# Kernel tuning notes

Hardware: AMD Instinct MI355X
Metric: run time of the kernel (lower is better)

Reference implementation:

```python
import jax, jax.numpy as jnp
import numpy as np

IN_CH = 256
OUT_CH = 256
RED = 4
QK = OUT_CH // RED  # 64


def setup_inputs() -> dict:
    key = jax.random.key(0)
    ks = jax.random.split(key, 7)
    s = 1.0 / np.sqrt(IN_CH)
    return {
        "x": jax.random.normal(ks[0], (8, IN_CH, 64, 64), dtype=jnp.float32),
        "w_q": jax.random.uniform(ks[1], (QK, IN_CH), jnp.float32, -s, s),
        "b_q": jax.random.uniform(ks[2], (QK,), jnp.float32, -s, s),
        "w_k": jax.random.uniform(ks[3], (QK, IN_CH), jnp.float32, -s, s),
        "b_k": jax.random.uniform(ks[4], (QK,), jnp.float32, -s, s),
        "w_v": jax.random.uniform(ks[5], (OUT_CH, IN_CH), jnp.float32, -s, s),
        "b_v": jax.random.uniform(ks[6], (OUT_CH,), jnp.float32, -s, s),
    }


def reference(x, w_q, b_q, w_k, b_k, w_v, b_v):
    B, C, H, W = x.shape
    xt = x.reshape(B, C, H * W)  # [B, C, N]
    # 1x1 convs == channel matmuls
    q = jnp.einsum('dc,bcn->bnd', w_q, xt) + b_q  # [B, N, QK]
    k = jnp.einsum('dc,bcn->bdn', w_k, xt) + b_k[:, None]  # [B, QK, N]
    v = jnp.einsum('dc,bcn->bnd', w_v, xt) + b_v  # [B, N, OUT]
    scores = jnp.einsum('bnd,bdm->bnm', q, k)  # [B, N, N], no scaling (as in source)
    attn = jax.nn.softmax(scores, axis=-1)
    out = jnp.einsum('bnm,bmd->bdn', attn, v)  # [B, OUT, N]
    return out.reshape(B, -1, H, W)
```

## Files before the change

### kernel.cpp

```cpp
#include <hip/hip_runtime.h>

typedef __bf16 bf16x8 __attribute__((ext_vector_type(8)));
typedef __bf16 bf16x2 __attribute__((ext_vector_type(2)));
typedef float f32x4 __attribute__((ext_vector_type(4)));
typedef unsigned int u32;
typedef u32 u32x4v __attribute__((ext_vector_type(4)));
typedef unsigned short u16;

#define LOG2E 1.44269504088896f

__device__ __forceinline__ u32 pk2(float a, float b){
  bf16x2 v; v[0] = (__bf16)a; v[1] = (__bf16)b;
  return __builtin_bit_cast(u32, v);
}

__global__ void prep_w(const float* __restrict__ wq, const float* __restrict__ wk,
                       const float* __restrict__ wv, u16* __restrict__ wfrag){
  int idx  = blockIdx.x * 256 + threadIdx.x;
  int e    = idx & 7;
  int lane = (idx >> 3) & 63;
  int f    = idx >> 9;
  int cc = f / 24, dt = f % 24;
  int d = dt * 16 + (lane & 15);
  int c = cc * 32 + (lane >> 4) * 8 + e;
  float v;
  if (d < 64)       v = wq[d * 256 + c];
  else if (d < 128) v = wk[(d - 64) * 256 + c];
  else              v = wv[(d - 128) * 256 + c];
  __bf16 h = (__bf16)v;
  wfrag[idx] = __builtin_bit_cast(u16, h);
}

__launch_bounds__(512, 4)
__global__ void proj_kernel(const float* __restrict__ x,
                            const float* __restrict__ bq, const float* __restrict__ bk,
                            const float* __restrict__ bv,
                            const u16* __restrict__ wfrag,
                            u16* __restrict__ qb, u16* __restrict__ kb, u16* __restrict__ vt)
{
  __shared__ u16 xlds[64 * 256];
  const int b    = blockIdx.x & 7;
  const int n0   = (blockIdx.x >> 3) * 64;
  const int t    = threadIdx.x;
  const int lane = t & 63;
  const int w    = t >> 6;
  const int g    = lane >> 4, j = lane & 15;

  {
    const int n  = t & 63;
    const int ch = t >> 6;
    const float* xp = x + ((size_t)b * 256) * 4096 + n0 + n;
    char* lbase = reinterpret_cast<char*>(xlds);
    #pragma unroll
    for (int pass = 0; pass < 4; ++pass){
      int c = pass * 64 + ch * 8;
      float f0 = xp[(size_t)(c+0)*4096], f1 = xp[(size_t)(c+1)*4096];
      float f2 = xp[(size_t)(c+2)*4096], f3 = xp[(size_t)(c+3)*4096];
      float f4 = xp[(size_t)(c+4)*4096], f5 = xp[(size_t)(c+5)*4096];
      float f6 = xp[(size_t)(c+6)*4096], f7 = xp[(size_t)(c+7)*4096];
      uint4 q;
      q.x = pk2(f0, f1); q.y = pk2(f2, f3); q.z = pk2(f4, f5); q.w = pk2(f6, f7);
      u32 off = (u32)n * 512 + (((u32)c * 2) ^ (((u32)n & 31) << 4));
      *reinterpret_cast<uint4*>(lbase + off) = q;
    }
  }
  __syncthreads();

  f32x4 acc[3][4];
  #pragma unroll
  for (int i = 0; i < 3; ++i)
    #pragma unroll
    for (int nt = 0; nt < 4; ++nt) acc[i][nt] = f32x4{0.f,0.f,0.f,0.f};

  const char* lbase = reinterpret_cast<const char*>(xlds);
  for (int cc = 0; cc < 8; ++cc){
    bf16x8 a[3];
    #pragma unroll
    for (int i = 0; i < 3; ++i)
      a[i] = *reinterpret_cast<const bf16x8*>(wfrag + ((size_t)(cc*24 + w*3 + i) * 64 + lane) * 8);
    bf16x8 bb[4];
    #pragma unroll
    for (int nt = 0; nt < 4; ++nt){
      const u32 row = nt * 16 + j;
      const u32 off = row * 512 + (((u32)(cc * 64 + g * 16)) ^ ((row & 31) << 4));
      bb[nt] = *reinterpret_cast<const bf16x8*>(lbase + off);
    }
    #pragma unroll
    for (int i = 0; i < 3; ++i)
      #pragma unroll
      for (int nt = 0; nt < 4; ++nt)
        acc[i][nt] = __builtin_amdgcn_mfma_f32_16x16x32_bf16(a[i], bb[nt], acc[i][nt], 0, 0, 0);
  }

  #pragma unroll
  for (int i = 0; i < 3; ++i){
    const int dt = w * 3 + i;
    const int d0 = dt * 16;
    const int dd = d0 + 4 * g;
    if (d0 < 64){
      float b0 = bq[dd], b1 = bq[dd+1], b2 = bq[dd+2], b3 = bq[dd+3];
      #pragma unroll
      for (int nt = 0; nt < 4; ++nt){
        const int n = n0 + nt * 16 + j;
        uint2 u;
        u.x = pk2((acc[i][nt][0] + b0) * LOG2E, (acc[i][nt][1] + b1) * LOG2E);
        u.y = pk2((acc[i][nt][2] + b2) * LOG2E, (acc[i][nt][3] + b3) * LOG2E);
        *reinterpret_cast<uint2*>(qb + ((size_t)b * 4096 + n) * 64 + dd) = u;
      }
    } else if (d0 < 128){
      const int dk = dd - 64;
      float b0 = bk[dk], b1 = bk[dk+1], b2 = bk[dk+2], b3 = bk[dk+3];
      #pragma unroll
      for (int nt = 0; nt < 4; ++nt){
        const int n = n0 + nt * 16 + j;
        uint2 u;
        u.x = pk2(acc[i][nt][0] + b0, acc[i][nt][1] + b1);
        u.y = pk2(acc[i][nt][2] + b2, acc[i][nt][3] + b3);
        *reinterpret_cast<uint2*>(kb + ((size_t)b * 4096 + n) * 64 + dk) = u;
      }
    } else {
      const int dv = dd - 128;
      float b0 = bv[dv], b1 = bv[dv+1], b2 = bv[dv+2], b3 = bv[dv+3];
      #pragma unroll
      for (int nt = 0; nt < 4; ++nt){
        const int scol = ((nt & 2) << 4) | ((j & 12) << 1) | ((nt & 1) << 2) | (j & 3);
        const int n = n0 + scol;
        u16* vp = vt + (size_t)b * 256 * 4096 + n;
        __bf16 h0 = (__bf16)(acc[i][nt][0] + b0);
        __bf16 h1 = (__bf16)(acc[i][nt][1] + b1);
        __bf16 h2 = (__bf16)(acc[i][nt][2] + b2);
        __bf16 h3 = (__bf16)(acc[i][nt][3] + b3);
        vp[(size_t)(dv+0) * 4096] = __builtin_bit_cast(u16, h0);
        vp[(size_t)(dv+1) * 4096] = __builtin_bit_cast(u16, h1);
        vp[(size_t)(dv+2) * 4096] = __builtin_bit_cast(u16, h2);
        vp[(size_t)(dv+3) * 4096] = __builtin_bit_cast(u16, h3);
      }
    }
  }
}

__launch_bounds__(512, 4)
__global__ void attn_kernel(const u16* __restrict__ qb, const u16* __restrict__ kb,
                            const u16* __restrict__ vt, float* __restrict__ out)
{
  __shared__ u16 kl[2][64 * 64];
  __shared__ u16 vl[2][256 * 64];

  const int b    = blockIdx.x & 7;
  const int qc   = blockIdx.x >> 3;
  const int t    = threadIdx.x, lane = t & 63, w = t >> 6;
  const int g    = lane >> 4, j = lane & 15;
  const int colq = w & 3;
  const int dvh  = (w >> 2) * 128;

  const u16* Kg = kb + (size_t)b * 4096 * 64;
  const u16* Vg = vt + (size_t)b * 256 * 4096;

  const u16* Qrow = qb + ((size_t)b * 4096 + qc * 64 + colq * 16 + j) * 64;
  const bf16x8 qf0 = *reinterpret_cast<const bf16x8*>(Qrow + 8 * g);
  const bf16x8 qf1 = *reinterpret_cast<const bf16x8*>(Qrow + 32 + 8 * g);

  f32x4 o[8];
  #pragma unroll
  for (int i = 0; i < 8; ++i) o[i] = f32x4{0.f,0.f,0.f,0.f};
  float mrun = -1.0e30f, lrun = 0.f;

  auto stage = [&](int tile, int buf){
    const int m0 = tile * 64;
    {
      const int r = w * 8 + (lane >> 3);
      const char* src = reinterpret_cast<const char*>(Kg + (size_t)(m0 + r) * 64)
                        + ((((u32)lane & 7) * 16) ^ ((((u32)r) & 7) << 4));
      char* dst = reinterpret_cast<char*>(&kl[buf][0]) + w * 1024;
      __builtin_amdgcn_global_load_lds((const __attribute__((address_space(1))) void*)src,
                                       (__attribute__((address_space(3))) void*)dst, 16, 0, 0);
    }
    #pragma unroll
    for (int i = 0; i < 4; ++i){
      const int dv = i * 64 + w * 8 + (lane >> 3);
      const char* src = reinterpret_cast<const char*>(Vg + (size_t)dv * 4096 + m0)
                        + ((((u32)lane & 7) * 16) ^ (((u32)dv & 7) << 4));
      char* dst = reinterpret_cast<char*>(&vl[buf][0]) + i * 8192 + w * 1024;
      __builtin_amdgcn_global_load_lds((const __attribute__((address_space(1))) void*)src,
                                       (__attribute__((address_space(3))) void*)dst, 16, 0, 0);
    }
  };

  stage(0, 0);
  __syncthreads();

  const u32 vsw = ((u32)j & 7) << 4;

  for (int tile = 0; tile < 64; ++tile){
    const int cur = tile & 1;
    if (tile + 1 < 64) stage(tile + 1, cur ^ 1);

    const char* kbase = reinterpret_cast<const char*>(&kl[cur][0]);
    const char* vbase = reinterpret_cast<const char*>(&vl[cur][0]);

    f32x4 s[4];
    __builtin_amdgcn_s_setprio(1);
    #pragma unroll
    for (int mt = 0; mt < 4; ++mt){
      const u32 row = mt * 16 + j;
      const u32 sw  = (row & 7) << 4;
      bf16x8 ka0 = *reinterpret_cast<const bf16x8*>(kbase + row * 128 + (((u32)(g * 16)) ^ sw));
      bf16x8 ka1 = *reinterpret_cast<const bf16x8*>(kbase + row * 128 + (((u32)(64 + g * 16)) ^ sw));
      f32x4 z = f32x4{0.f,0.f,0.f,0.f};
      z = __builtin_amdgcn_mfma_f32_16x16x32_bf16(ka0, qf0, z, 0, 0, 0);
      z = __builtin_amdgcn_mfma_f32_16x16x32_bf16(ka1, qf1, z, 0, 0, 0);
      s[mt] = z;
    }
    __builtin_amdgcn_s_setprio(0);

    float pmax = s[0][0];
    #pragma unroll
    for (int mt = 0; mt < 4; ++mt)
      #pragma unroll
      for (int r = 0; r < 4; ++r) pmax = fmaxf(pmax, s[mt][r]);
    pmax = fmaxf(pmax, __shfl_xor(pmax, 16));
    pmax = fmaxf(pmax, __shfl_xor(pmax, 32));

    if (__any(pmax > mrun + 8.0f)){
      const float mnew  = fmaxf(mrun, pmax);
      const float alpha = __builtin_amdgcn_exp2f(mrun - mnew);
      mrun = mnew;
      lrun *= alpha;
      #pragma unroll
      for (int i = 0; i < 8; ++i){
        o[i][0] *= alpha; o[i][1] *= alpha; o[i][2] *= alpha; o[i][3] *= alpha;
      }
    }

    float psum = 0.f;
    u32 pw[8];
    #pragma unroll
    for (int mt = 0; mt < 4; ++mt){
      float p0 = __builtin_amdgcn_exp2f(s[mt][0] - mrun);
      float p1 = __builtin_amdgcn_exp2f(s[mt][1] - mrun);
      float p2 = __builtin_amdgcn_exp2f(s[mt][2] - mrun);
      float p3 = __builtin_amdgcn_exp2f(s[mt][3] - mrun);
      psum += (p0 + p1) + (p2 + p3);
      pw[2*mt]   = pk2(p0, p1);
      pw[2*mt+1] = pk2(p2, p3);
    }
    psum += __shfl_xor(psum, 16);
    psum += __shfl_xor(psum, 32);
    lrun += psum;

    __builtin_amdgcn_s_setprio(1);
    #pragma unroll
    for (int mc = 0; mc < 2; ++mc){
      u32x4v pv = { pw[4*mc+0], pw[4*mc+1], pw[4*mc+2], pw[4*mc+3] };
      bf16x8 pf = __builtin_bit_cast(bf16x8, pv);
      #pragma unroll
      for (int dt = 0; dt < 8; ++dt){
        const u32 dv = dvh + dt * 16 + j;
        bf16x8 vf = *reinterpret_cast<const bf16x8*>(vbase + dv * 128 + (((u32)(mc * 64 + 16 * g)) ^ vsw));
        o[dt] = __builtin_amdgcn_mfma_f32_16x16x32_bf16(vf, pf, o[dt], 0, 0, 0);
      }
    }
    __builtin_amdgcn_s_setprio(0);

    __syncthreads();
  }

  const float rinv = 1.0f / lrun;
  const int n = qc * 64 + colq * 16 + j;
  float* ob = out + (size_t)b * 256 * 4096 + n;
  #pragma unroll
  for (int dt = 0; dt < 8; ++dt){
    const int dv0 = dvh + dt * 16 + 4 * g;
    #pragma unroll
    for (int r = 0; r < 4; ++r)
      ob[(size_t)(dv0 + r) * 4096] = o[dt][r] * rinv;
  }
}

extern "C" void kernel_launch(void* const* d_in, const int* in_sizes, int n_in,
                              void* d_out, int out_size, void* d_ws, size_t ws_size,
                              hipStream_t stream)
{
  (void)in_sizes; (void)n_in; (void)out_size; (void)ws_size;
  const float* x  = (const float*)d_in[0];
  const float* wq = (const float*)d_in[1];
  const float* bq = (const float*)d_in[2];
  const float* wk = (const float*)d_in[3];
  const float* bk = (const float*)d_in[4];
  const float* wv = (const float*)d_in[5];
  const float* bv = (const float*)d_in[6];
  float* out = (float*)d_out;

  char* ws = (char*)d_ws;
  u16* qbuf  = (u16*)(ws + 0);
  u16* kbuf  = (u16*)(ws + 4194304);
  u16* vbuf  = (u16*)(ws + 8388608);
  u16* wfrag = (u16*)(ws + 25165824);

  prep_w<<<dim3(384), dim3(256), 0, stream>>>(wq, wk, wv, wfrag);
  proj_kernel<<<dim3(512), dim3(512), 0, stream>>>(x, bq, bk, bv, wfrag, qbuf, kbuf, vbuf);
  attn_kernel<<<dim3(512), dim3(512), 0, stream>>>(qbuf, kbuf, vbuf, out);
}
```

Measured before the change: 228.8 us.

## Switch attention kernel to 32x32x16 MFMA tiles with four waves per block

Rewrites the attention kernel to use 32x32x16 bf16 MFMAs instead of 16x16x32. Each of four waves now owns 32 query columns by 128 value channels, where before eight waves each owned 16 columns. The V column permutation written by the projection kernel is changed to match the new P fragment layout. The aim is higher MFMA throughput per instruction and fewer LDS fragment reads per FLOP, at the cost of more accumulator registers per thread and fewer waves per block.

```diff
diff --git a/kernel.cpp b/kernel.cpp
--- a/kernel.cpp
+++ b/kernel.cpp
@@ -3,6 +3,7 @@
 typedef __bf16 bf16x8 __attribute__((ext_vector_type(8)));
 typedef __bf16 bf16x2 __attribute__((ext_vector_type(2)));
 typedef float f32x4 __attribute__((ext_vector_type(4)));
+typedef float f32x16 __attribute__((ext_vector_type(16)));
 typedef unsigned int u32;
 typedef u32 u32x4v __attribute__((ext_vector_type(4)));
 typedef unsigned short u16;
@@ -123,7 +124,7 @@
       float b0 = bv[dv], b1 = bv[dv+1], b2 = bv[dv+2], b3 = bv[dv+3];
       #pragma unroll
       for (int nt = 0; nt < 4; ++nt){
-        const int scol = ((nt & 2) << 4) | ((j & 12) << 1) | ((nt & 1) << 2) | (j & 3);
+        const int scol = (nt << 4) | ((j & 8) >> 1) | ((j & 4) << 1) | (j & 3);
         const int n = n0 + scol;
         u16* vp = vt + (size_t)b * 256 * 4096 + n;
         __bf16 h0 = (__bf16)(acc[i][nt][0] + b0);
@@ -139,7 +140,7 @@
   }
 }
 
-__launch_bounds__(512, 4)
+__launch_bounds__(256, 2)
 __global__ void attn_kernel(const u16* __restrict__ qb, const u16* __restrict__ kb,
                             const u16* __restrict__ vt, float* __restrict__ out)
 {
@@ -149,38 +150,43 @@
   const int b    = blockIdx.x & 7;
   const int qc   = blockIdx.x >> 3;
   const int t    = threadIdx.x, lane = t & 63, w = t >> 6;
-  const int g    = lane >> 4, j = lane & 15;
-  const int colq = w & 3;
-  const int dvh  = (w >> 2) * 128;
+  const int i32l = lane & 31, hi = lane >> 5;
+  const int colg = w & 1;
+  const int dvh  = (w >> 1) * 128;
 
   const u16* Kg = kb + (size_t)b * 4096 * 64;
   const u16* Vg = vt + (size_t)b * 256 * 4096;
 
-  const u16* Qrow = qb + ((size_t)b * 4096 + qc * 64 + colq * 16 + j) * 64;
-  const bf16x8 qf0 = *reinterpret_cast<const bf16x8*>(Qrow + 8 * g);
-  const bf16x8 qf1 = *reinterpret_cast<const bf16x8*>(Qrow + 32 + 8 * g);
-
-  f32x4 o[8];
-  #pragma unroll
-  for (int i = 0; i < 8; ++i) o[i] = f32x4{0.f,0.f,0.f,0.f};
+  const u16* Qrow = qb + ((size_t)b * 4096 + qc * 64 + colg * 32 + i32l) * 64;
+  bf16x8 qf[4];
+  #pragma unroll
+  for (int kc = 0; kc < 4; ++kc)
+    qf[kc] = *reinterpret_cast<const bf16x8*>(Qrow + kc * 16 + hi * 8);
+
+  f32x16 o[4];
+  #pragma unroll
+  for (int ds = 0; ds < 4; ++ds)
+    #pragma unroll
+    for (int r = 0; r < 16; ++r) o[ds][r] = 0.f;
   float mrun = -1.0e30f, lrun = 0.f;
 
   auto stage = [&](int tile, int buf){
     const int m0 = tile * 64;
-    {
-      const int r = w * 8 + (lane >> 3);
+    #pragma unroll
+    for (int i = 0; i < 2; ++i){
+      const int r = i * 32 + w * 8 + (lane >> 3);
       const char* src = reinterpret_cast<const char*>(Kg + (size_t)(m0 + r) * 64)
                         + ((((u32)lane & 7) * 16) ^ ((((u32)r) & 7) << 4));
-      char* dst = reinterpret_cast<char*>(&kl[buf][0]) + w * 1024;
+      char* dst = reinterpret_cast<char*>(&kl[buf][0]) + i * 4096 + w * 1024;
       __builtin_amdgcn_global_load_lds((const __attribute__((address_space(1))) void*)src,
                                        (__attribute__((address_space(3))) void*)dst, 16, 0, 0);
     }
     #pragma unroll
-    for (int i = 0; i < 4; ++i){
-      const int dv = i * 64 + w * 8 + (lane >> 3);
+    for (int i = 0; i < 8; ++i){
+      const int dv = i * 32 + w * 8 + (lane >> 3);
       const char* src = reinterpret_cast<const char*>(Vg + (size_t)dv * 4096 + m0)
                         + ((((u32)lane & 7) * 16) ^ (((u32)dv & 7) << 4));
-      char* dst = reinterpret_cast<char*>(&vl[buf][0]) + i * 8192 + w * 1024;
+      char* dst = reinterpret_cast<char*>(&vl[buf][0]) + i * 4096 + w * 1024;
       __builtin_amdgcn_global_load_lds((const __attribute__((address_space(1))) void*)src,
                                        (__attribute__((address_space(3))) void*)dst, 16, 0, 0);
     }
@@ -189,7 +195,8 @@
   stage(0, 0);
   __syncthreads();
 
-  const u32 vsw = ((u32)j & 7) << 4;
+  const u32 swk   = ((u32)i32l & 7) << 4;
+  const u32 r0off = (u32)i32l * 128;
 
   for (int tile = 0; tile < 64; ++tile){
     const int cur = tile & 1;
@@ -198,27 +205,26 @@
     const char* kbase = reinterpret_cast<const char*>(&kl[cur][0]);
     const char* vbase = reinterpret_cast<const char*>(&vl[cur][0]);
 
-    f32x4 s[4];
+    f32x16 s0, s1;
+    #pragma unroll
+    for (int r = 0; r < 16; ++r){ s0[r] = 0.f; s1[r] = 0.f; }
     __builtin_amdgcn_s_setprio(1);
     #pragma unroll
-    for (int mt = 0; mt < 4; ++mt){
-      const u32 row = mt * 16 + j;
-      const u32 sw  = (row & 7) << 4;
-      bf16x8 ka0 = *reinterpret_cast<const bf16x8*>(kbase + row * 128 + (((u32)(g * 16)) ^ sw));
-      bf16x8 ka1 = *reinterpret_cast<const bf16x8*>(kbase + row * 128 + (((u32)(64 + g * 16)) ^ sw));
-      f32x4 z = f32x4{0.f,0.f,0.f,0.f};
-      z = __builtin_amdgcn_mfma_f32_16x16x32_bf16(ka0, qf0, z, 0, 0, 0);
-      z = __builtin_amdgcn_mfma_f32_16x16x32_bf16(ka1, qf1, z, 0, 0, 0);
-      s[mt] = z;
+    for (int kc = 0; kc < 4; ++kc){
+      const u32 cb = ((u32)(kc * 32 + hi * 16)) ^ swk;
+      bf16x8 ka0 = *reinterpret_cast<const bf16x8*>(kbase + r0off + cb);
+      bf16x8 ka1 = *reinterpret_cast<const bf16x8*>(kbase + 4096 + r0off + cb);
+      s0 = __builtin_amdgcn_mfma_f32_32x32x16_bf16(ka0, qf[kc], s0, 0, 0, 0);
+      s1 = __builtin_amdgcn_mfma_f32_32x32x16_bf16(ka1, qf[kc], s1, 0, 0, 0);
     }
     __builtin_amdgcn_s_setprio(0);
 
-    float pmax = s[0][0];
-    #pragma unroll
-    for (int mt = 0; mt < 4; ++mt)
-      #pragma unroll
-      for (int r = 0; r < 4; ++r) pmax = fmaxf(pmax, s[mt][r]);
-    pmax = fmaxf(pmax, __shfl_xor(pmax, 16));
+    float mx[8];
+    #pragma unroll
+    for (int r = 0; r < 8; ++r)
+      mx[r] = fmaxf(fmaxf(s0[r], s0[r+8]), fmaxf(s1[r], s1[r+8]));
+    float pmax = fmaxf(fmaxf(fmaxf(mx[0],mx[1]), fmaxf(mx[2],mx[3])),
+                       fmaxf(fmaxf(mx[4],mx[5]), fmaxf(mx[6],mx[7])));
     pmax = fmaxf(pmax, __shfl_xor(pmax, 32));
 
     if (__any(pmax > mrun + 8.0f)){
@@ -227,53 +233,57 @@
       mrun = mnew;
       lrun *= alpha;
       #pragma unroll
-      for (int i = 0; i < 8; ++i){
-        o[i][0] *= alpha; o[i][1] *= alpha; o[i][2] *= alpha; o[i][3] *= alpha;
+      for (int ds = 0; ds < 4; ++ds)
+        #pragma unroll
+        for (int r = 0; r < 16; ++r) o[ds][r] *= alpha;
+    }
+
+    float p0[16], p1[16];
+    #pragma unroll
+    for (int r = 0; r < 16; ++r){
+      p0[r] = __builtin_amdgcn_exp2f(s0[r] - mrun);
+      p1[r] = __builtin_amdgcn_exp2f(s1[r] - mrun);
+    }
+    float a8[8];
+    #pragma unroll
+    for (int r = 0; r < 8; ++r) a8[r] = (p0[r] + p0[r+8]) + (p1[r] + p1[r+8]);
+    float ps = ((a8[0]+a8[1]) + (a8[2]+a8[3])) + ((a8[4]+a8[5]) + (a8[6]+a8[7]));
+    ps += __shfl_xor(ps, 32);
+    lrun += ps;
+
+    u32x4v w0 = { pk2(p0[0],p0[1]),  pk2(p0[2],p0[3]),  pk2(p0[4],p0[5]),  pk2(p0[6],p0[7]) };
+    u32x4v w1 = { pk2(p0[8],p0[9]),  pk2(p0[10],p0[11]),pk2(p0[12],p0[13]),pk2(p0[14],p0[15]) };
+    u32x4v w2 = { pk2(p1[0],p1[1]),  pk2(p1[2],p1[3]),  pk2(p1[4],p1[5]),  pk2(p1[6],p1[7]) };
+    u32x4v w3 = { pk2(p1[8],p1[9]),  pk2(p1[10],p1[11]),pk2(p1[12],p1[13]),pk2(p1[14],p1[15]) };
+    bf16x8 pf[4] = { __builtin_bit_cast(bf16x8, w0), __builtin_bit_cast(bf16x8, w1),
+                     __builtin_bit_cast(bf16x8, w2), __builtin_bit_cast(bf16x8, w3) };
+
+    __builtin_amdgcn_s_setprio(1);
+    #pragma unroll
+    for (int c = 0; c < 4; ++c){
+      const u32 cb = ((u32)(c * 32 + hi * 16)) ^ swk;
+      #pragma unroll
+      for (int ds = 0; ds < 4; ++ds){
+        const u32 voff = (u32)(dvh + ds * 32) * 128 + r0off + cb;
+        bf16x8 vf = *reinterpret_cast<const bf16x8*>(vbase + voff);
+        o[ds] = __builtin_amdgcn_mfma_f32_32x32x16_bf16(vf, pf[c], o[ds], 0, 0, 0);
       }
     }
-
-    float psum = 0.f;
-    u32 pw[8];
-    #pragma unroll
-    for (int mt = 0; mt < 4; ++mt){
-      float p0 = __builtin_amdgcn_exp2f(s[mt][0] - mrun);
-      float p1 = __builtin_amdgcn_exp2f(s[mt][1] - mrun);
-      float p2 = __builtin_amdgcn_exp2f(s[mt][2] - mrun);
-      float p3 = __builtin_amdgcn_exp2f(s[mt][3] - mrun);
-      psum += (p0 + p1) + (p2 + p3);
-      pw[2*mt]   = pk2(p0, p1);
-      pw[2*mt+1] = pk2(p2, p3);
-    }
-    psum += __shfl_xor(psum, 16);
-    psum += __shfl_xor(psum, 32);
-    lrun += psum;
-
-    __builtin_amdgcn_s_setprio(1);
-    #pragma unroll
-    for (int mc = 0; mc < 2; ++mc){
-      u32x4v pv = { pw[4*mc+0], pw[4*mc+1], pw[4*mc+2], pw[4*mc+3] };
-      bf16x8 pf = __builtin_bit_cast(bf16x8, pv);
-      #pragma unroll
-      for (int dt = 0; dt < 8; ++dt){
-        const u32 dv = dvh + dt * 16 + j;
-        bf16x8 vf = *reinterpret_cast<const bf16x8*>(vbase + dv * 128 + (((u32)(mc * 64 + 16 * g)) ^ vsw));
-        o[dt] = __builtin_amdgcn_mfma_f32_16x16x32_bf16(vf, pf, o[dt], 0, 0, 0);
-      }
-    }
     __builtin_amdgcn_s_setprio(0);
 
     __syncthreads();
   }
 
   const float rinv = 1.0f / lrun;
-  const int n = qc * 64 + colq * 16 + j;
+  const int n = qc * 64 + colg * 32 + i32l;
   float* ob = out + (size_t)b * 256 * 4096 + n;
   #pragma unroll
-  for (int dt = 0; dt < 8; ++dt){
-    const int dv0 = dvh + dt * 16 + 4 * g;
-    #pragma unroll
-    for (int r = 0; r < 4; ++r)
-      ob[(size_t)(dv0 + r) * 4096] = o[dt][r] * rinv;
+  for (int ds = 0; ds < 4; ++ds){
+    #pragma unroll
+    for (int r = 0; r < 16; ++r){
+      const int dv = dvh + ds * 32 + (r & 3) + 8 * (r >> 2) + 4 * hi;
+      ob[(size_t)dv * 4096] = o[ds][r] * rinv;
+    }
   }
 }
 
@@ -299,5 +309,5 @@
 
   prep_w<<<dim3(384), dim3(256), 0, stream>>>(wq, wk, wv, wfrag);
   proj_kernel<<<dim3(512), dim3(512), 0, stream>>>(x, bq, bk, bv, wfrag, qbuf, kbuf, vbuf);
-  attn_kernel<<<dim3(512), dim3(512), 0, stream>>>(qbuf, kbuf, vbuf, out);
-}
+  attn_kernel<<<dim3(512), dim3(256), 0, stream>>>(qbuf, kbuf, vbuf, out);
+}
```

After: 227.6 us. Within noise of the previous version (-0.5%).
